# Kernel tuning notes

Measured on AMD Instinct MI355X. Metric: run time of the kernel, lower is better.

## Reference

```python
import jax, jax.numpy as jnp
import numpy as np

B = 256      # graph pairs
NPG = 28     # nodes per graph
MAXN = 32    # max_node_set_size
EPG = 64     # edges per graph (== max_edge_set_size, so no edge padding)
MAXE = 64
D = 128      # node_state_dim
FN = 32      # raw node feature dim
FE = 32      # raw edge feature dim
SK = 64      # sinkhorn_feature_dim
STEPS = 3    # propagation_steps
TEMP = 0.1
ITERS = 20
CW = 0.9     # consistency_weight
G = 2 * B
N = G * NPG
E = G * EPG


def _lin(key, fi, fo):
    return jax.random.normal(key, (fi, fo), jnp.float32) / np.sqrt(fi)


def setup_inputs() -> dict:
    key = jax.random.key(0)
    ks = jax.random.split(key, 12)
    rng = np.random.default_rng(0)
    off = (np.arange(G) * NPG)[:, None]   # graphs ordered q0,c0,q1,c1,...
    from_idx = jnp.asarray((rng.integers(0, NPG, (G, EPG)) + off).reshape(-1), jnp.int32)
    to_idx = jnp.asarray((rng.integers(0, NPG, (G, EPG)) + off).reshape(-1), jnp.int32)
    return dict(
        node_features=jax.random.normal(ks[0], (N, FN), jnp.float32),
        edge_features=jax.random.normal(ks[1], (E, FE), jnp.float32),
        enc_nw=_lin(ks[2], FN, D), enc_nb=jnp.zeros((D,), jnp.float32),
        enc_ew=_lin(ks[3], FE, D), enc_eb=jnp.zeros((D,), jnp.float32),
        msg_w1=_lin(ks[4], 3 * D, 2 * D), msg_b1=jnp.zeros((2 * D,), jnp.float32),
        msg_w2=_lin(ks[5], 2 * D, D), msg_b2=jnp.zeros((D,), jnp.float32),
        rmsg_w1=_lin(ks[6], 3 * D, 2 * D), rmsg_b1=jnp.zeros((2 * D,), jnp.float32),
        rmsg_w2=_lin(ks[7], 2 * D, D), rmsg_b2=jnp.zeros((D,), jnp.float32),
        upd_w1=_lin(ks[8], 2 * D, 2 * D), upd_b1=jnp.zeros((2 * D,), jnp.float32),
        upd_w2=_lin(ks[9], 2 * D, D), upd_b2=jnp.zeros((D,), jnp.float32),
        sk_w1=_lin(ks[10], D, SK), sk_b1=jnp.zeros((SK,), jnp.float32),
        sk_w2=_lin(ks[11], SK, SK), sk_b2=jnp.zeros((SK,), jnp.float32),
        from_idx=from_idx, to_idx=to_idx,
        query_sizes=jnp.full((B,), NPG, jnp.int32),
        corpus_sizes=jnp.full((B,), NPG, jnp.int32),
    )


def _mlp2(x, w1, b1, w2, b2):
    return jnp.maximum(x @ w1 + b1, 0.0) @ w2 + b2


def _sinkhorn(log_alpha):
    # log-domain sinkhorn (noise_factor = 0 -> deterministic)
    la = log_alpha / TEMP
    for _ in range(ITERS):
        la = la - jax.nn.logsumexp(la, axis=2, keepdims=True)
        la = la - jax.nn.logsumexp(la, axis=1, keepdims=True)
    return jnp.exp(la)


def _align(q, c, plan):
    # feature_alignment_score: -relu(q - P @ c).sum over set and feature dims
    return -jnp.maximum(q - plan @ c, 0.0).sum(axis=(1, 2))


def _forward(node_features, edge_features, enc_nw, enc_nb, enc_ew, enc_eb,
             msg_w1, msg_b1, msg_w2, msg_b2, rmsg_w1, rmsg_b1, rmsg_w2, rmsg_b2,
             upd_w1, upd_b1, upd_w2, upd_b2, sk_w1, sk_b1, sk_w2, sk_b2,
             from_idx, to_idx, query_sizes, corpus_sizes):
    h = node_features @ enc_nw + enc_nb        # encoder, [N, D]
    e = edge_features @ enc_ew + enc_eb        # [E, D]

    def messages(h):
        f = _mlp2(jnp.concatenate([h[from_idx], h[to_idx], e], -1), msg_w1, msg_b1, msg_w2, msg_b2)
        r = _mlp2(jnp.concatenate([h[to_idx], h[from_idx], e], -1), rmsg_w1, rmsg_b1, rmsg_w2, rmsg_b2)
        return f, r

    for _ in range(STEPS):  # GraphPropLayer x propagation_steps
        f, r = messages(h)
        agg = jax.ops.segment_sum(f, to_idx, num_segments=N) + \
              jax.ops.segment_sum(r, from_idx, num_segments=N)
        h = h + _mlp2(jnp.concatenate([agg, h], -1), upd_w1, upd_b1, upd_w2, upd_b2)

    # split_and_stack nodes: graphs alternate query/corpus, pad NPG -> MAXN
    hs = jnp.pad(h.reshape(B, 2, NPG, D), ((0, 0), (0, 0), (0, MAXN - NPG), (0, 0)))
    q_nodes, c_nodes = hs[:, 0], hs[:, 1]      # [B, MAXN, D]

    tq = _mlp2(q_nodes, sk_w1, sk_b1, sk_w2, sk_b2)
    tc = _mlp2(c_nodes, sk_w1, sk_b1, sk_w2, sk_b2)
    pos = jnp.arange(MAXN)[None, :]
    mq = tq * (pos < query_sizes[:, None])[..., None]
    mc = tc * (pos < corpus_sizes[:, None])[..., None]
    node_plan = _sinkhorn(jnp.einsum('bqd,bcd->bqc', mq, mc))   # [B, MAXN, MAXN]

    # propagation_messages on final node states
    f, r = messages(h)
    em = (f + r).reshape(B, 2, EPG, D)         # EPG == MAXE -> no pad
    q_edges, c_edges = em[:, 0], em[:, 1]

    # local (within-graph) endpoint indices for kronecker lookup
    fl = (from_idx % NPG).reshape(B, 2, EPG)
    tl = (to_idx % NPG).reshape(B, 2, EPG)
    qf, cf = fl[:, 0], fl[:, 1]
    qt, ct = tl[:, 0], tl[:, 1]

    def kron(T, qf, qt, cf, ct):
        straight = T[qf][:, cf] * T[qt][:, ct]   # [MAXE, MAXE]
        cross = T[qf][:, ct] * T[qt][:, cf]
        return straight + cross

    edge_scores = jax.vmap(kron)(node_plan, qf, qt, cf, ct)     # [B, MAXE, MAXE]
    edge_plan = _sinkhorn(edge_scores)

    return _align(q_nodes, c_nodes, node_plan) + CW * _align(q_edges, c_edges, edge_plan)


def reference(node_features, edge_features, enc_nw, enc_nb, enc_ew, enc_eb,
              msg_w1, msg_b1, msg_w2, msg_b2, rmsg_w1, rmsg_b1, rmsg_w2, rmsg_b2,
              upd_w1, upd_b1, upd_w2, upd_b2, sk_w1, sk_b1, sk_w2, sk_b2,
              from_idx, to_idx, query_sizes, corpus_sizes):
    return _forward(node_features, edge_features, enc_nw, enc_nb, enc_ew, enc_eb,
                    msg_w1, msg_b1, msg_w2, msg_b2, rmsg_w1, rmsg_b1, rmsg_w2, rmsg_b2,
                    upd_w1, upd_b1, upd_w2, upd_b2, sk_w1, sk_b1, sk_w2, sk_b2,
                    from_idx, to_idx, query_sizes, corpus_sizes)
```

## Files before the change

### kernel.cpp

```cpp
#include <hip/hip_runtime.h>
#include <math.h>

#define NPG 28
#define EPG 64
#define NB  256
#define NG  512
#define NN  14336
#define NE  32768
#define TEMPINV 10.0f
#define SINK_ITERS 20
#define CW 0.9f

typedef unsigned int uint;
typedef unsigned short ushort;
typedef __attribute__((ext_vector_type(8))) __bf16 bf16x8;
typedef __attribute__((ext_vector_type(4))) float f32x4;

__device__ __forceinline__ ushort f2bf(float x) {
    uint u = __float_as_uint(x);
    u += 0x7fffu + ((u >> 16) & 1u);
    return (ushort)(u >> 16);
}
__device__ __forceinline__ uint f2bf2(float lo, float hi) {
    return (uint)f2bf(lo) | ((uint)f2bf(hi) << 16);
}
__device__ __forceinline__ float bflo(uint w) { return __uint_as_float(w << 16); }
__device__ __forceinline__ float bfhi(uint w) { return __uint_as_float(w & 0xffff0000u); }
__device__ __forceinline__ uint relu_sum_pk(uint w1, uint w2, uint w3) {
    float lo = fmaxf(bflo(w1) + bflo(w2) + bflo(w3), 0.f);
    float hi = fmaxf(bfhi(w1) + bfhi(w2) + bfhi(w3), 0.f);
    return f2bf2(lo, hi);
}
__device__ __forceinline__ uint4 pack_f32x8(const float* src) {
    const float4 f0 = *(const float4*)src;
    const float4 f1 = *(const float4*)(src + 4);
    uint4 o;
    o.x = f2bf2(f0.x, f0.y);
    o.y = f2bf2(f0.z, f0.w);
    o.z = f2bf2(f1.x, f1.y);
    o.w = f2bf2(f1.z, f1.w);
    return o;
}
__device__ __forceinline__ f32x4 mfma16(bf16x8 a, bf16x8 b, f32x4 c) {
    return __builtin_amdgcn_mfma_f32_16x16x32_bf16(a, b, c, 0, 0, 0);
}

__global__ __launch_bounds__(512, 1) void gnn_fused(
    const float* __restrict__ nf, const float* __restrict__ ef,
    const ushort* __restrict__ encL, const float* __restrict__ enc_nb,
    const ushort* __restrict__ WcombL, const float* __restrict__ bcomb,
    const ushort* __restrict__ WhpL,
    const ushort* __restrict__ W2fL, const ushort* __restrict__ W2rL,
    const float* __restrict__ b2f, const float* __restrict__ b2r,
    const ushort* __restrict__ UW1T, const float* __restrict__ ub1,
    const ushort* __restrict__ UW2T, const float* __restrict__ ub2,
    const int* __restrict__ from_idx, const int* __restrict__ to_idx,
    float* __restrict__ h, float* __restrict__ EM)
{
    __shared__ ushort HPs[NPG * 520];
    __shared__ ushort ECs[2 * 8 * 2048];
    __shared__ float acc_s[NPG * 132];
    __shared__ float hs[NPG * 132];
    __shared__ int fl[64], tl[64];
    const int g = blockIdx.x;
    const int tid = threadIdx.x;
    const int w = tid >> 6, lane = tid & 63;
    const int li = lane & 15, quad = lane >> 4;
    const int wm = w >> 1, wn = w & 1;
    ushort* hid = &HPs[0];

    if (tid < 64) {
        fl[tid] = from_idx[g * 64 + tid] - g * NPG;
        tl[tid] = to_idx[g * 64 + tid] - g * NPG;
    }

    {
        uint4 anf[2];
#pragma unroll
        for (int mi = 0; mi < 2; ++mi) {
            const int row = mi * 16 + li;
            const int rr = (row < NPG) ? row : 0;
            const float4 f0 = *(const float4*)(nf + ((size_t)g * NPG + rr) * 32 + quad * 8);
            const float4 f1 = *(const float4*)(nf + ((size_t)g * NPG + rr) * 32 + quad * 8 + 4);
            uint4 o;
            o.x = f2bf2(f0.x, f0.y); o.y = f2bf2(f0.z, f0.w);
            o.z = f2bf2(f1.x, f1.y); o.w = f2bf2(f1.z, f1.w);
            anf[mi] = o;
        }
        const int col = w * 16 + li;
        const bf16x8 b = __builtin_bit_cast(bf16x8,
            *(const uint4*)(encL + (size_t)col * 32 + quad * 8));
        f32x4 c0 = mfma16(__builtin_bit_cast(bf16x8, anf[0]), b, f32x4{0.f, 0.f, 0.f, 0.f});
        f32x4 c1 = mfma16(__builtin_bit_cast(bf16x8, anf[1]), b, f32x4{0.f, 0.f, 0.f, 0.f});
        const float bv = enc_nb[col];
#pragma unroll
        for (int r = 0; r < 4; ++r) {
            const int r0 = quad * 4 + r;
            hs[r0 * 132 + col] = c0[r] + bv;
            const int r1 = 16 + quad * 4 + r;
            if (r1 < NPG) hs[r1 * 132 + col] = c1[r] + bv;
        }
    }
    {
        uint4 aef[4];
#pragma unroll
        for (int mi = 0; mi < 4; ++mi) {
            const int e = mi * 16 + li;
            const float4 f0 = *(const float4*)(ef + ((size_t)g * 64 + e) * 32 + quad * 8);
            const float4 f1 = *(const float4*)(ef + ((size_t)g * 64 + e) * 32 + quad * 8 + 4);
            uint4 o;
            o.x = f2bf2(f0.x, f0.y); o.y = f2bf2(f0.z, f0.w);
            o.z = f2bf2(f1.x, f1.y); o.w = f2bf2(f1.z, f1.w);
            aef[mi] = o;
        }
#pragma unroll
        for (int ni = 0; ni < 4; ++ni) {
            const int col = w * 64 + ni * 16 + li;
            const bf16x8 b = __builtin_bit_cast(bf16x8,
                *(const uint4*)(WcombL + (size_t)col * 32 + quad * 8));
            const float bv = bcomb[col];
            const int pp = col >> 8, kbl = (col >> 5) & 7, j = col & 31;
#pragma unroll
            for (int mi = 0; mi < 4; ++mi) {
                f32x4 c = mfma16(__builtin_bit_cast(bf16x8, aef[mi]), b,
                                 f32x4{0.f, 0.f, 0.f, 0.f});
#pragma unroll
                for (int r = 0; r < 4; ++r) {
                    const int e = mi * 16 + quad * 4 + r;
                    ECs[pp * 16384 + kbl * 2048 + e * 32 + j] = f2bf(c[r] + bv);
                }
            }
        }
    }
    __syncthreads();

#pragma unroll 1
    for (int step = 0; step < 3; ++step) {
        uint4 ha[2][4];
#pragma unroll
        for (int mi = 0; mi < 2; ++mi) {
            const int row = mi * 16 + li;
            const int rr = (row < NPG) ? row : 0;
#pragma unroll
            for (int kb = 0; kb < 4; ++kb)
                ha[mi][kb] = pack_f32x8(&hs[rr * 132 + kb * 32 + quad * 8]);
        }
        for (int u = tid; u < NPG * 132; u += 512) acc_s[u] = 0.f;

        f32x4 acc[4];
#pragma unroll
        for (int j = 0; j < 4; ++j) acc[j] = f32x4{0.f, 0.f, 0.f, 0.f};

#pragma unroll 1
        for (int p = 0; p < 2; ++p) {
            {
                const int colw = w * 64;
#pragma unroll
                for (int ni = 0; ni < 4; ++ni) {
                    const int col = colw + ni * 16 + li;
                    const ushort* pb = WhpL + (size_t)(p * 512 + col) * 32 + quad * 8;
                    f32x4 c0 = f32x4{0.f, 0.f, 0.f, 0.f};
                    f32x4 c1 = f32x4{0.f, 0.f, 0.f, 0.f};
#pragma unroll
                    for (int kb = 0; kb < 4; ++kb) {
                        const bf16x8 b = __builtin_bit_cast(bf16x8,
                            *(const uint4*)(pb + (size_t)kb * 32768));
                        c0 = mfma16(__builtin_bit_cast(bf16x8, ha[0][kb]), b, c0);
                        c1 = mfma16(__builtin_bit_cast(bf16x8, ha[1][kb]), b, c1);
                    }
#pragma unroll
                    for (int r = 0; r < 4; ++r) {
                        const int r0 = quad * 4 + r;
                        HPs[r0 * 520 + col] = f2bf(c0[r]);
                        const int r1 = 16 + quad * 4 + r;
                        if (r1 < NPG) HPs[r1 * 520 + col] = f2bf(c1[r]);
                    }
                }
            }
            __syncthreads();

            if (p == 1) {
#pragma unroll
                for (int j = 0; j < 4; ++j) acc[j] = f32x4{0.f, 0.f, 0.f, 0.f};
            }
            const int e = wm * 16 + li;
            const int i1 = p ? tl[e] : fl[e];
            const int i2 = p ? fl[e] : tl[e];
            const int ad1 = i1 * 520 + quad * 8;
            const int ad2 = i2 * 520 + 256 + quad * 8;
            const int ade = p * 16384 + e * 32 + quad * 8;
            const ushort* W2L = p ? W2rL : W2fL;
            const int n0 = wn * 64;
            const ushort* pb[4];
#pragma unroll
            for (int ni = 0; ni < 4; ++ni)
                pb[ni] = W2L + (size_t)(n0 + ni * 16 + li) * 32 + quad * 8;
#pragma unroll
            for (int kb = 0; kb < 8; ++kb) {
                const uint4 u1 = *(const uint4*)&HPs[ad1 + kb * 32];
                const uint4 u2 = *(const uint4*)&HPs[ad2 + kb * 32];
                const uint4 ue = *(const uint4*)&ECs[ade + kb * 2048];
                uint4 o;
                o.x = relu_sum_pk(u1.x, u2.x, ue.x);
                o.y = relu_sum_pk(u1.y, u2.y, ue.y);
                o.z = relu_sum_pk(u1.z, u2.z, ue.z);
                o.w = relu_sum_pk(u1.w, u2.w, ue.w);
                const bf16x8 a = __builtin_bit_cast(bf16x8, o);
#pragma unroll
                for (int ni = 0; ni < 4; ++ni) {
                    const bf16x8 b = __builtin_bit_cast(bf16x8,
                        *(const uint4*)(pb[ni] + (size_t)kb * 4096));
                    acc[ni] = mfma16(a, b, acc[ni]);
                }
            }
            {
                const int* targ = p ? fl : tl;
                const float* bias = p ? b2r : b2f;
                float bv[4];
#pragma unroll
                for (int ni = 0; ni < 4; ++ni) bv[ni] = bias[n0 + ni * 16 + li];
#pragma unroll
                for (int r = 0; r < 4; ++r) {
                    const int loc = targ[wm * 16 + quad * 4 + r];
#pragma unroll
                    for (int ni = 0; ni < 4; ++ni)
                        atomicAdd(&acc_s[loc * 132 + n0 + ni * 16 + li],
                                  acc[ni][r] + bv[ni]);
                }
            }
            __syncthreads();
        }

        {
            const int n0u = w * 32;
            f32x4 ua[2][2];
#pragma unroll
            for (int mi = 0; mi < 2; ++mi)
#pragma unroll
                for (int ni = 0; ni < 2; ++ni) ua[mi][ni] = f32x4{0.f, 0.f, 0.f, 0.f};
            const ushort* pb0 = UW1T + (size_t)(n0u + li) * 256 + quad * 8;
            const ushort* pb1 = UW1T + (size_t)(n0u + 16 + li) * 256 + quad * 8;
#pragma unroll
            for (int kb = 0; kb < 8; ++kb) {
                bf16x8 a[2];
                if (kb < 4) {
#pragma unroll
                    for (int mi = 0; mi < 2; ++mi) {
                        const int row = mi * 16 + li;
                        const int rr = (row < NPG) ? row : 0;
                        a[mi] = __builtin_bit_cast(bf16x8,
                            pack_f32x8(&acc_s[rr * 132 + kb * 32 + quad * 8]));
                    }
                } else {
                    a[0] = __builtin_bit_cast(bf16x8, ha[0][kb - 4]);
                    a[1] = __builtin_bit_cast(bf16x8, ha[1][kb - 4]);
                }
                const bf16x8 b0 = __builtin_bit_cast(bf16x8, *(const uint4*)(pb0 + kb * 32));
                const bf16x8 b1 = __builtin_bit_cast(bf16x8, *(const uint4*)(pb1 + kb * 32));
#pragma unroll
                for (int mi = 0; mi < 2; ++mi) {
                    ua[mi][0] = mfma16(a[mi], b0, ua[mi][0]);
                    ua[mi][1] = mfma16(a[mi], b1, ua[mi][1]);
                }
            }
            const float bv0 = ub1[n0u + li], bv1 = ub1[n0u + 16 + li];
#pragma unroll
            for (int mi = 0; mi < 2; ++mi)
#pragma unroll
                for (int r = 0; r < 4; ++r) {
                    const int row = mi * 16 + quad * 4 + r;
                    if (row < NPG) {
                        hid[row * 264 + n0u + li] = f2bf(fmaxf(ua[mi][0][r] + bv0, 0.f));
                        hid[row * 264 + n0u + 16 + li] = f2bf(fmaxf(ua[mi][1][r] + bv1, 0.f));
                    }
                }
        }
        __syncthreads();
        {
            const int n0u = w * 16;
            f32x4 ua[2];
            ua[0] = f32x4{0.f, 0.f, 0.f, 0.f};
            ua[1] = f32x4{0.f, 0.f, 0.f, 0.f};
            const ushort* pb0 = UW2T + (size_t)(n0u + li) * 256 + quad * 8;
#pragma unroll
            for (int kb = 0; kb < 8; ++kb) {
                bf16x8 a[2];
#pragma unroll
                for (int mi = 0; mi < 2; ++mi) {
                    const int row = mi * 16 + li;
                    const int rr = (row < NPG) ? row : 0;
                    a[mi] = __builtin_bit_cast(bf16x8,
                        *(const uint4*)&hid[rr * 264 + kb * 32 + quad * 8]);
                }
                const bf16x8 b0 = __builtin_bit_cast(bf16x8, *(const uint4*)(pb0 + kb * 32));
                ua[0] = mfma16(a[0], b0, ua[0]);
                ua[1] = mfma16(a[1], b0, ua[1]);
            }
            const float bv = ub2[n0u + li];
#pragma unroll
            for (int mi = 0; mi < 2; ++mi)
#pragma unroll
                for (int r = 0; r < 4; ++r) {
                    const int row = mi * 16 + quad * 4 + r;
                    if (row < NPG)
                        hs[row * 132 + n0u + li] += ua[mi][r] + bv;
                }
        }
        __syncthreads();
    }

    {
        uint4 ha[2][4];
#pragma unroll
        for (int mi = 0; mi < 2; ++mi) {
            const int row = mi * 16 + li;
            const int rr = (row < NPG) ? row : 0;
#pragma unroll
            for (int kb = 0; kb < 4; ++kb)
                ha[mi][kb] = pack_f32x8(&hs[rr * 132 + kb * 32 + quad * 8]);
        }
        f32x4 acc[4];
#pragma unroll
        for (int j = 0; j < 4; ++j) acc[j] = f32x4{0.f, 0.f, 0.f, 0.f};
        const int n0 = wn * 64;
#pragma unroll 1
        for (int p = 0; p < 2; ++p) {
            {
                const int colw = w * 64;
#pragma unroll
                for (int ni = 0; ni < 4; ++ni) {
                    const int col = colw + ni * 16 + li;
                    const ushort* pb = WhpL + (size_t)(p * 512 + col) * 32 + quad * 8;
                    f32x4 c0 = f32x4{0.f, 0.f, 0.f, 0.f};
                    f32x4 c1 = f32x4{0.f, 0.f, 0.f, 0.f};
#pragma unroll
                    for (int kb = 0; kb < 4; ++kb) {
                        const bf16x8 b = __builtin_bit_cast(bf16x8,
                            *(const uint4*)(pb + (size_t)kb * 32768));
                        c0 = mfma16(__builtin_bit_cast(bf16x8, ha[0][kb]), b, c0);
                        c1 = mfma16(__builtin_bit_cast(bf16x8, ha[1][kb]), b, c1);
                    }
#pragma unroll
                    for (int r = 0; r < 4; ++r) {
                        const int r0 = quad * 4 + r;
                        HPs[r0 * 520 + col] = f2bf(c0[r]);
                        const int r1 = 16 + quad * 4 + r;
                        if (r1 < NPG) HPs[r1 * 520 + col] = f2bf(c1[r]);
                    }
                }
            }
            __syncthreads();
            const int e = wm * 16 + li;
            const int i1 = p ? tl[e] : fl[e];
            const int i2 = p ? fl[e] : tl[e];
            const int ad1 = i1 * 520 + quad * 8;
            const int ad2 = i2 * 520 + 256 + quad * 8;
            const int ade = p * 16384 + e * 32 + quad * 8;
            const ushort* W2L = p ? W2rL : W2fL;
            const ushort* pb[4];
#pragma unroll
            for (int ni = 0; ni < 4; ++ni)
                pb[ni] = W2L + (size_t)(n0 + ni * 16 + li) * 32 + quad * 8;
#pragma unroll
            for (int kb = 0; kb < 8; ++kb) {
                const uint4 u1 = *(const uint4*)&HPs[ad1 + kb * 32];
                const uint4 u2 = *(const uint4*)&HPs[ad2 + kb * 32];
                const uint4 ue = *(const uint4*)&ECs[ade + kb * 2048];
                uint4 o;
                o.x = relu_sum_pk(u1.x, u2.x, ue.x);
                o.y = relu_sum_pk(u1.y, u2.y, ue.y);
                o.z = relu_sum_pk(u1.z, u2.z, ue.z);
                o.w = relu_sum_pk(u1.w, u2.w, ue.w);
                const bf16x8 a = __builtin_bit_cast(bf16x8, o);
#pragma unroll
                for (int ni = 0; ni < 4; ++ni) {
                    const bf16x8 b = __builtin_bit_cast(bf16x8,
                        *(const uint4*)(pb[ni] + (size_t)kb * 4096));
                    acc[ni] = mfma16(a, b, acc[ni]);
                }
            }
            __syncthreads();
        }
        float bv[4];
#pragma unroll
        for (int ni = 0; ni < 4; ++ni)
            bv[ni] = b2f[n0 + ni * 16 + li] + b2r[n0 + ni * 16 + li];
#pragma unroll
        for (int r = 0; r < 4; ++r) {
            const int erow = g * 64 + wm * 16 + quad * 4 + r;
#pragma unroll
            for (int ni = 0; ni < 4; ++ni)
                EM[(size_t)erow * 128 + n0 + ni * 16 + li] = acc[ni][r] + bv[ni];
        }
    }
    for (int u = tid; u < NPG * 128; u += 512)
        h[(size_t)g * (NPG * 128) + u] = hs[(u >> 7) * 132 + (u & 127)];
}

__global__ __launch_bounds__(256) void pack2(
    const float* __restrict__ msg_w1, const float* __restrict__ rmsg_w1,
    const float* __restrict__ msg_b1, const float* __restrict__ rmsg_b1,
    const float* __restrict__ enc_ew, const float* __restrict__ enc_eb,
    const float* __restrict__ enc_nw,
    const float* __restrict__ msg_w2, const float* __restrict__ rmsg_w2,
    const float* __restrict__ upd_w1, const float* __restrict__ upd_w2,
    ushort* __restrict__ WcombL, float* __restrict__ bcomb,
    ushort* __restrict__ encL,
    ushort* __restrict__ WhpL, ushort* __restrict__ W2fL, ushort* __restrict__ W2rL,
    ushort* __restrict__ UW1T, ushort* __restrict__ UW2T)
{
    const int gid = blockIdx.x, tid = threadIdx.x;
    if (gid < 64) {
        const int idx = gid * 256 + tid;
        const int a = idx >> 9, n = idx & 511;
        const float* Wsrc = (n < 256) ? msg_w1 : rmsg_w1;
        const int nc = n & 255;
        float s = 0.f;
        for (int j = 0; j < 128; ++j)
            s = fmaf(enc_ew[a * 128 + j], Wsrc[(256 + j) * 256 + nc], s);
        WcombL[n * 32 + a] = f2bf(s);
    } else if (gid < 66) {
        const int n = (gid - 64) * 256 + tid;
        const float* Wsrc = (n < 256) ? msg_w1 : rmsg_w1;
        const float* bsrc = (n < 256) ? msg_b1 : rmsg_b1;
        const int nc = n & 255;
        float s = bsrc[nc];
        for (int j = 0; j < 128; ++j)
            s = fmaf(enc_eb[j], Wsrc[(256 + j) * 256 + nc], s);
        bcomb[n] = s;
    } else if (gid < 82) {
        const int idx = (gid - 66) * 256 + tid;
        const int n = idx >> 5, k = idx & 31;
        encL[idx] = f2bf(enc_nw[k * 128 + n]);
    } else if (gid < 594) {
        const int idx = (gid - 82) * 256 + tid;
        const int n = idx >> 7, k = idx & 127;
        const float* Wsrc = (n < 512) ? msg_w1 : rmsg_w1;
        const int part = (n >> 8) & 1, col = n & 255;
        WhpL[(size_t)(k >> 5) * 32768 + n * 32 + (k & 31)] =
            f2bf(Wsrc[(part * 128 + k) * 256 + col]);
    } else if (gid < 722) {
        const int idx = (gid - 594) * 256 + tid;
        const int n = idx >> 8, k = idx & 255;
        W2fL[(size_t)(k >> 5) * 4096 + n * 32 + (k & 31)] = f2bf(msg_w2[k * 128 + n]);
    } else if (gid < 850) {
        const int idx = (gid - 722) * 256 + tid;
        const int n = idx >> 8, k = idx & 255;
        W2rL[(size_t)(k >> 5) * 4096 + n * 32 + (k & 31)] = f2bf(rmsg_w2[k * 128 + n]);
    } else if (gid < 1106) {
        const int idx = (gid - 850) * 256 + tid;
        const int n = idx >> 8, k = idx & 255;
        UW1T[idx] = f2bf(upd_w1[k * 256 + n]);
    } else {
        const int idx = (gid - 1106) * 256 + tid;
        const int n = idx >> 8, k = idx & 255;
        UW2T[idx] = f2bf(upd_w2[k * 128 + n]);
    }
}

__global__ __launch_bounds__(256) void node_kernel(
    const float* __restrict__ h,
    const float* __restrict__ w1, const float* __restrict__ b1,
    const float* __restrict__ w2, const float* __restrict__ b2,
    const int* __restrict__ qsz, const int* __restrict__ csz,
    float* __restrict__ plan_out, float* __restrict__ loss_out)
{
    __shared__ float qn[32][128];
    __shared__ float cn[32][128];
    __shared__ float t1[32][64];
    __shared__ float mq[32][68];
    __shared__ float mc[32][68];
    __shared__ float la[32][33];
    __shared__ float red[4];
    const int bb = blockIdx.x;
    const int tid = threadIdx.x;
    const int qs = qsz[bb], cs = csz[bb];
    for (int u = tid * 4; u < 4096; u += 1024) {
        const int p = u >> 7, d = u & 127;
        float4 zq = make_float4(0.f, 0.f, 0.f, 0.f), zc = zq;
        if (p < NPG) {
            zq = *(const float4*)(h + (size_t)((2 * bb) * NPG + p) * 128 + d);
            zc = *(const float4*)(h + (size_t)((2 * bb + 1) * NPG + p) * 128 + d);
        }
        *(float4*)&qn[p][d] = zq;
        *(float4*)&cn[p][d] = zc;
    }
    __syncthreads();
    const int col = tid & 63;
    const int rg  = tid >> 6;
    for (int s = 0; s < 2; ++s) {
        const float (*src)[128] = s ? cn : qn;
        float (*dst)[68] = s ? mc : mq;
        const int sz = s ? cs : qs;
        float a8[8];
#pragma unroll
        for (int u = 0; u < 8; ++u) a8[u] = b1[col];
        for (int k = 0; k < 128; ++k) {
            const float wv = w1[k * 64 + col];
#pragma unroll
            for (int u = 0; u < 8; ++u) a8[u] = fmaf(src[rg + 4 * u][k], wv, a8[u]);
        }
#pragma unroll
        for (int u = 0; u < 8; ++u) t1[rg + 4 * u][col] = fmaxf(a8[u], 0.f);
        __syncthreads();
#pragma unroll
        for (int u = 0; u < 8; ++u) a8[u] = b2[col];
        for (int k = 0; k < 64; ++k) {
            const float wv = w2[k * 64 + col];
#pragma unroll
            for (int u = 0; u < 8; ++u) a8[u] = fmaf(t1[rg + 4 * u][k], wv, a8[u]);
        }
#pragma unroll
        for (int u = 0; u < 8; ++u) {
            const int r = rg + 4 * u;
            dst[r][col] = (r < sz) ? a8[u] : 0.f;
        }
        __syncthreads();
    }
    {
        const int q = tid >> 3, cg = tid & 7;
#pragma unroll
        for (int u = 0; u < 4; ++u) {
            const int c = cg + 8 * u;
            float s = 0.f;
            for (int d = 0; d < 64; ++d) s = fmaf(mq[q][d], mc[c][d], s);
            la[q][c] = s * TEMPINV;
        }
    }
    __syncthreads();
    const int l8 = tid & 7, rq = tid >> 3;
    for (int it = 0; it < SINK_ITERS; ++it) {
        {
            float x[4];
#pragma unroll
            for (int u = 0; u < 4; ++u) x[u] = la[rq][l8 * 4 + u];
            float m = fmaxf(fmaxf(x[0], x[1]), fmaxf(x[2], x[3]));
            m = fmaxf(m, __shfl_xor(m, 1));
            m = fmaxf(m, __shfl_xor(m, 2));
            m = fmaxf(m, __shfl_xor(m, 4));
            float s = __expf(x[0] - m) + __expf(x[1] - m) + __expf(x[2] - m) + __expf(x[3] - m);
            s += __shfl_xor(s, 1);
            s += __shfl_xor(s, 2);
            s += __shfl_xor(s, 4);
            const float lse = m + __logf(s);
#pragma unroll
            for (int u = 0; u < 4; ++u) la[rq][l8 * 4 + u] = x[u] - lse;
        }
        __syncthreads();
        {
            float x[4];
#pragma unroll
            for (int u = 0; u < 4; ++u) x[u] = la[l8 * 4 + u][rq];
            float m = fmaxf(fmaxf(x[0], x[1]), fmaxf(x[2], x[3]));
            m = fmaxf(m, __shfl_xor(m, 1));
            m = fmaxf(m, __shfl_xor(m, 2));
            m = fmaxf(m, __shfl_xor(m, 4));
            float s = __expf(x[0] - m) + __expf(x[1] - m) + __expf(x[2] - m) + __expf(x[3] - m);
            s += __shfl_xor(s, 1);
            s += __shfl_xor(s, 2);
            s += __shfl_xor(s, 4);
            const float lse = m + __logf(s);
#pragma unroll
            for (int u = 0; u < 4; ++u) la[l8 * 4 + u][rq] = x[u] - lse;
        }
        __syncthreads();
    }
    for (int u = tid; u < 1024; u += 256) {
        const int q = u >> 5, c = u & 31;
        const float p = __expf(la[q][c]);
        la[q][c] = p;
        plan_out[(size_t)bb * 1024 + u] = p;
    }
    __syncthreads();
    float lsum = 0.f;
    {
        const int q = tid >> 3, dg = tid & 7;
        for (int u = 0; u < 16; ++u) {
            const int d = dg + 8 * u;
            float pc = 0.f;
#pragma unroll
            for (int c = 0; c < 32; ++c) pc = fmaf(la[q][c], cn[c][d], pc);
            lsum += fmaxf(qn[q][d] - pc, 0.f);
        }
    }
#pragma unroll
    for (int off = 1; off < 64; off <<= 1) lsum += __shfl_xor(lsum, off);
    if ((tid & 63) == 0) red[tid >> 6] = lsum;
    __syncthreads();
    if (tid == 0) loss_out[bb] = -(red[0] + red[1] + red[2] + red[3]);
}

__global__ __launch_bounds__(256) void edge_kernel(
    const float* __restrict__ plan, const float* __restrict__ EM,
    const int* __restrict__ from_idx, const int* __restrict__ to_idx,
    float* __restrict__ loss_out)
{
    __shared__ float T[32][33];
    __shared__ float la[64][65];
    __shared__ float ce[64][128];
    __shared__ int qf[64], qt[64], cfi[64], cti[64];
    __shared__ float red[4];
    const int bb = blockIdx.x;
    const int tid = threadIdx.x;
    for (int u = tid; u < 1024; u += 256) T[u >> 5][u & 31] = plan[(size_t)bb * 1024 + u];
    if (tid < 64) {
        const int gq = 2 * bb, gc = 2 * bb + 1;
        qf[tid]  = from_idx[gq * 64 + tid] - gq * NPG;
        qt[tid]  = to_idx  [gq * 64 + tid] - gq * NPG;
        cfi[tid] = from_idx[gc * 64 + tid] - gc * NPG;
        cti[tid] = to_idx  [gc * 64 + tid] - gc * NPG;
    }
    {
        const int gc = 2 * bb + 1;
        for (int u = tid * 4; u < 8192; u += 1024) {
            const int i = u >> 7, d = u & 127;
            *(float4*)&ce[i][d] = *(const float4*)(EM + (size_t)(gc * 64 + i) * 128 + d);
        }
    }
    __syncthreads();
    {
        const int i = tid >> 2, jg = tid & 3;
        const int a = qf[i], b_ = qt[i];
#pragma unroll
        for (int u = 0; u < 16; ++u) {
            const int j = jg * 16 + u;
            const float s = T[a][cfi[j]] * T[b_][cti[j]] + T[a][cti[j]] * T[b_][cfi[j]];
            la[i][j] = s * TEMPINV;
        }
    }
    __syncthreads();
    const int l4 = tid & 3, rr = tid >> 2;
    for (int it = 0; it < SINK_ITERS; ++it) {
        {
            float x[16];
#pragma unroll
            for (int u = 0; u < 16; ++u) x[u] = la[rr][l4 * 16 + u];
            float m = x[0];
#pragma unroll
            for (int u = 1; u < 16; ++u) m = fmaxf(m, x[u]);
            m = fmaxf(m, __shfl_xor(m, 1));
            m = fmaxf(m, __shfl_xor(m, 2));
            float s = 0.f;
#pragma unroll
            for (int u = 0; u < 16; ++u) s += __expf(x[u] - m);
            s += __shfl_xor(s, 1);
            s += __shfl_xor(s, 2);
            const float lse = m + __logf(s);
#pragma unroll
            for (int u = 0; u < 16; ++u) la[rr][l4 * 16 + u] = x[u] - lse;
        }
        __syncthreads();
        {
            float x[16];
#pragma unroll
            for (int u = 0; u < 16; ++u) x[u] = la[l4 * 16 + u][rr];
            float m = x[0];
#pragma unroll
            for (int u = 1; u < 16; ++u) m = fmaxf(m, x[u]);
            m = fmaxf(m, __shfl_xor(m, 1));
            m = fmaxf(m, __shfl_xor(m, 2));
            float s = 0.f;
#pragma unroll
            for (int u = 0; u < 16; ++u) s += __expf(x[u] - m);
            s += __shfl_xor(s, 1);
            s += __shfl_xor(s, 2);
            const float lse = m + __logf(s);
#pragma unroll
            for (int u = 0; u < 16; ++u) la[l4 * 16 + u][rr] = x[u] - lse;
        }
        __syncthreads();
    }
    for (int u = tid; u < 4096; u += 256) la[u >> 6][u & 63] = __expf(la[u >> 6][u & 63]);
    __syncthreads();
    float lsum = 0.f;
    {
        const int q = tid >> 2, dg = tid & 3;
        const float* qe = EM + (size_t)((2 * bb) * 64 + q) * 128;
        for (int u = 0; u < 32; ++u) {
            const int d = dg + 4 * u;
            float pc = 0.f;
            for (int c = 0; c < 64; ++c) pc = fmaf(la[q][c], ce[c][d], pc);
            lsum += fmaxf(qe[d] - pc, 0.f);
        }
    }
#pragma unroll
    for (int off = 1; off < 64; off <<= 1) lsum += __shfl_xor(lsum, off);
    if ((tid & 63) == 0) red[tid >> 6] = lsum;
    __syncthreads();
    if (tid == 0) loss_out[bb] -= CW * (red[0] + red[1] + red[2] + red[3]);
}

extern "C" void kernel_launch(void* const* d_in, const int* in_sizes, int n_in,
                              void* d_out, int out_size, void* d_ws, size_t ws_size,
                              hipStream_t stream)
{
    const float* node_features = (const float*)d_in[0];
    const float* edge_features = (const float*)d_in[1];
    const float* enc_nw  = (const float*)d_in[2];
    const float* enc_nb  = (const float*)d_in[3];
    const float* enc_ew  = (const float*)d_in[4];
    const float* enc_eb  = (const float*)d_in[5];
    const float* msg_w1  = (const float*)d_in[6];
    const float* msg_b1  = (const float*)d_in[7];
    const float* msg_w2  = (const float*)d_in[8];
    const float* msg_b2  = (const float*)d_in[9];
    const float* rmsg_w1 = (const float*)d_in[10];
    const float* rmsg_b1 = (const float*)d_in[11];
    const float* rmsg_w2 = (const float*)d_in[12];
    const float* rmsg_b2 = (const float*)d_in[13];
    const float* upd_w1  = (const float*)d_in[14];
    const float* upd_b1  = (const float*)d_in[15];
    const float* upd_w2  = (const float*)d_in[16];
    const float* upd_b2  = (const float*)d_in[17];
    const float* sk_w1   = (const float*)d_in[18];
    const float* sk_b1   = (const float*)d_in[19];
    const float* sk_w2   = (const float*)d_in[20];
    const float* sk_b2   = (const float*)d_in[21];
    const int* from_idx  = (const int*)d_in[22];
    const int* to_idx    = (const int*)d_in[23];
    const int* qsizes    = (const int*)d_in[24];
    const int* csizes    = (const int*)d_in[25];
    float* out = (float*)d_out;

    float* ws     = (float*)d_ws;
    float* h      = ws;
    float* EM     = h + (size_t)NN * 128;
    float* plan   = EM + (size_t)NE * 128;
    float* bcomb  = plan + (size_t)NB * 1024;
    ushort* WcombL = (ushort*)(bcomb + 512);
    ushort* encL  = WcombL + 16384;
    ushort* WhpL  = encL + 4096;
    ushort* W2fL  = WhpL + 131072;
    ushort* W2rL  = W2fL + 32768;
    ushort* UW1T  = W2rL + 32768;
    ushort* UW2T  = UW1T + 65536;

    const dim3 blk(256);
    const dim3 blk512(512);

    pack2<<<1234, blk, 0, stream>>>(msg_w1, rmsg_w1, msg_b1, rmsg_b1,
                                    enc_ew, enc_eb, enc_nw, msg_w2, rmsg_w2,
                                    upd_w1, upd_w2,
                                    WcombL, bcomb, encL, WhpL, W2fL, W2rL, UW1T, UW2T);

    gnn_fused<<<dim3(NG), blk512, 0, stream>>>(
        node_features, edge_features, encL, enc_nb, WcombL, bcomb,
        WhpL, W2fL, W2rL, msg_b2, rmsg_b2,
        UW1T, upd_b1, UW2T, upd_b2, from_idx, to_idx, h, EM);

    node_kernel<<<NB, blk, 0, stream>>>(
        h, sk_w1, sk_b1, sk_w2, sk_b2, qsizes, csizes, plan, out);
    edge_kernel<<<NB, blk, 0, stream>>>(
        plan, EM, from_idx, to_idx, out);
}
```

Before: 467.5 us.

## Halve fused GNN block to 256 threads and keep edge-encoder output in registers

The fused GNN kernel now runs 256 threads per graph instead of 512, with each wave covering twice as many output columns, and launch bounds are set to allow two blocks per CU. The edge-encoder projections no longer sit in a dedicated 64KB shared buffer. They are computed through the reused HPs buffer and loaded once into per-thread registers (ecf) for all propagation steps. The aim is to cut shared memory use so more blocks fit per CU and to drop repeated LDS reads of edge terms. The cost is more registers per thread (8 accumulators plus 16 uint4 of edge data) and less parallelism within each block.

```diff
diff --git a/kernel.cpp b/kernel.cpp
--- a/kernel.cpp
+++ b/kernel.cpp
@@ -45,7 +45,7 @@
     return __builtin_amdgcn_mfma_f32_16x16x32_bf16(a, b, c, 0, 0, 0);
 }
 
-__global__ __launch_bounds__(512, 1) void gnn_fused(
+__global__ __launch_bounds__(256, 2) void gnn_fused(
     const float* __restrict__ nf, const float* __restrict__ ef,
     const ushort* __restrict__ encL, const float* __restrict__ enc_nb,
     const ushort* __restrict__ WcombL, const float* __restrict__ bcomb,
@@ -57,8 +57,7 @@
     const int* __restrict__ from_idx, const int* __restrict__ to_idx,
     float* __restrict__ h, float* __restrict__ EM)
 {
-    __shared__ ushort HPs[NPG * 520];
-    __shared__ ushort ECs[2 * 8 * 2048];
+    __shared__ ushort HPs[16640];
     __shared__ float acc_s[NPG * 132];
     __shared__ float hs[NPG * 132];
     __shared__ int fl[64], tl[64];
@@ -66,7 +65,6 @@
     const int tid = threadIdx.x;
     const int w = tid >> 6, lane = tid & 63;
     const int li = lane & 15, quad = lane >> 4;
-    const int wm = w >> 1, wn = w & 1;
     ushort* hid = &HPs[0];
 
     if (tid < 64) {
@@ -87,20 +85,25 @@
             o.z = f2bf2(f1.x, f1.y); o.w = f2bf2(f1.z, f1.w);
             anf[mi] = o;
         }
-        const int col = w * 16 + li;
-        const bf16x8 b = __builtin_bit_cast(bf16x8,
-            *(const uint4*)(encL + (size_t)col * 32 + quad * 8));
-        f32x4 c0 = mfma16(__builtin_bit_cast(bf16x8, anf[0]), b, f32x4{0.f, 0.f, 0.f, 0.f});
-        f32x4 c1 = mfma16(__builtin_bit_cast(bf16x8, anf[1]), b, f32x4{0.f, 0.f, 0.f, 0.f});
-        const float bv = enc_nb[col];
-#pragma unroll
-        for (int r = 0; r < 4; ++r) {
-            const int r0 = quad * 4 + r;
-            hs[r0 * 132 + col] = c0[r] + bv;
-            const int r1 = 16 + quad * 4 + r;
-            if (r1 < NPG) hs[r1 * 132 + col] = c1[r] + bv;
-        }
-    }
+#pragma unroll
+        for (int ni = 0; ni < 2; ++ni) {
+            const int col = w * 32 + ni * 16 + li;
+            const bf16x8 b = __builtin_bit_cast(bf16x8,
+                *(const uint4*)(encL + (size_t)col * 32 + quad * 8));
+            f32x4 c0 = mfma16(__builtin_bit_cast(bf16x8, anf[0]), b, f32x4{0.f, 0.f, 0.f, 0.f});
+            f32x4 c1 = mfma16(__builtin_bit_cast(bf16x8, anf[1]), b, f32x4{0.f, 0.f, 0.f, 0.f});
+            const float bv = enc_nb[col];
+#pragma unroll
+            for (int r = 0; r < 4; ++r) {
+                const int r0 = quad * 4 + r;
+                hs[r0 * 132 + col] = c0[r] + bv;
+                const int r1 = 16 + quad * 4 + r;
+                if (r1 < NPG) hs[r1 * 132 + col] = c1[r] + bv;
+            }
+        }
+    }
+
+    uint4 ecf[2][8];
     {
         uint4 aef[4];
 #pragma unroll
@@ -113,26 +116,35 @@
             o.z = f2bf2(f1.x, f1.y); o.w = f2bf2(f1.z, f1.w);
             aef[mi] = o;
         }
-#pragma unroll
-        for (int ni = 0; ni < 4; ++ni) {
-            const int col = w * 64 + ni * 16 + li;
-            const bf16x8 b = __builtin_bit_cast(bf16x8,
-                *(const uint4*)(WcombL + (size_t)col * 32 + quad * 8));
-            const float bv = bcomb[col];
-            const int pp = col >> 8, kbl = (col >> 5) & 7, j = col & 31;
-#pragma unroll
-            for (int mi = 0; mi < 4; ++mi) {
-                f32x4 c = mfma16(__builtin_bit_cast(bf16x8, aef[mi]), b,
-                                 f32x4{0.f, 0.f, 0.f, 0.f});
-#pragma unroll
-                for (int r = 0; r < 4; ++r) {
-                    const int e = mi * 16 + quad * 4 + r;
-                    ECs[pp * 16384 + kbl * 2048 + e * 32 + j] = f2bf(c[r] + bv);
-                }
-            }
-        }
-    }
-    __syncthreads();
+#pragma unroll 1
+        for (int p = 0; p < 2; ++p) {
+#pragma unroll
+            for (int ni = 0; ni < 4; ++ni) {
+                const int col = w * 64 + ni * 16 + li;
+                const int wcol = p * 256 + col;
+                const bf16x8 b = __builtin_bit_cast(bf16x8,
+                    *(const uint4*)(WcombL + (size_t)wcol * 32 + quad * 8));
+                const float bv = bcomb[wcol];
+                const int kbl = col >> 5, j = col & 31;
+#pragma unroll
+                for (int mi = 0; mi < 4; ++mi) {
+                    f32x4 c = mfma16(__builtin_bit_cast(bf16x8, aef[mi]), b,
+                                     f32x4{0.f, 0.f, 0.f, 0.f});
+#pragma unroll
+                    for (int r = 0; r < 4; ++r) {
+                        const int e = mi * 16 + quad * 4 + r;
+                        HPs[kbl * 2048 + e * 32 + j] = f2bf(c[r] + bv);
+                    }
+                }
+            }
+            __syncthreads();
+            const int eb = (w * 16 + li) * 32 + quad * 8;
+#pragma unroll
+            for (int kb = 0; kb < 8; ++kb)
+                ecf[p][kb] = *(const uint4*)&HPs[kb * 2048 + eb];
+            __syncthreads();
+        }
+    }
 
 #pragma unroll 1
     for (int step = 0; step < 3; ++step) {
@@ -145,18 +157,14 @@
             for (int kb = 0; kb < 4; ++kb)
                 ha[mi][kb] = pack_f32x8(&hs[rr * 132 + kb * 32 + quad * 8]);
         }
-        for (int u = tid; u < NPG * 132; u += 512) acc_s[u] = 0.f;
-
-        f32x4 acc[4];
-#pragma unroll
-        for (int j = 0; j < 4; ++j) acc[j] = f32x4{0.f, 0.f, 0.f, 0.f};
+        for (int u = tid; u < NPG * 132; u += 256) acc_s[u] = 0.f;
 
 #pragma unroll 1
         for (int p = 0; p < 2; ++p) {
             {
-                const int colw = w * 64;
-#pragma unroll
-                for (int ni = 0; ni < 4; ++ni) {
+                const int colw = w * 128;
+#pragma unroll
+                for (int ni = 0; ni < 8; ++ni) {
                     const int col = colw + ni * 16 + li;
                     const ushort* pb = WhpL + (size_t)(p * 512 + col) * 32 + quad * 8;
                     f32x4 c0 = f32x4{0.f, 0.f, 0.f, 0.f};
@@ -179,27 +187,20 @@
             }
             __syncthreads();
 
-            if (p == 1) {
-#pragma unroll
-                for (int j = 0; j < 4; ++j) acc[j] = f32x4{0.f, 0.f, 0.f, 0.f};
-            }
-            const int e = wm * 16 + li;
+            const int e = w * 16 + li;
             const int i1 = p ? tl[e] : fl[e];
             const int i2 = p ? fl[e] : tl[e];
             const int ad1 = i1 * 520 + quad * 8;
             const int ad2 = i2 * 520 + 256 + quad * 8;
-            const int ade = p * 16384 + e * 32 + quad * 8;
             const ushort* W2L = p ? W2rL : W2fL;
-            const int n0 = wn * 64;
-            const ushort* pb[4];
-#pragma unroll
-            for (int ni = 0; ni < 4; ++ni)
-                pb[ni] = W2L + (size_t)(n0 + ni * 16 + li) * 32 + quad * 8;
+            f32x4 acc[8];
+#pragma unroll
+            for (int j = 0; j < 8; ++j) acc[j] = f32x4{0.f, 0.f, 0.f, 0.f};
 #pragma unroll
             for (int kb = 0; kb < 8; ++kb) {
                 const uint4 u1 = *(const uint4*)&HPs[ad1 + kb * 32];
                 const uint4 u2 = *(const uint4*)&HPs[ad2 + kb * 32];
-                const uint4 ue = *(const uint4*)&ECs[ade + kb * 2048];
+                const uint4 ue = ecf[p][kb];
                 uint4 o;
                 o.x = relu_sum_pk(u1.x, u2.x, ue.x);
                 o.y = relu_sum_pk(u1.y, u2.y, ue.y);
@@ -207,24 +208,25 @@
                 o.w = relu_sum_pk(u1.w, u2.w, ue.w);
                 const bf16x8 a = __builtin_bit_cast(bf16x8, o);
 #pragma unroll
-                for (int ni = 0; ni < 4; ++ni) {
+                for (int ni = 0; ni < 8; ++ni) {
                     const bf16x8 b = __builtin_bit_cast(bf16x8,
-                        *(const uint4*)(pb[ni] + (size_t)kb * 4096));
+                        *(const uint4*)(W2L + (size_t)(ni * 16 + li) * 32 +
+                                        quad * 8 + (size_t)kb * 4096));
                     acc[ni] = mfma16(a, b, acc[ni]);
                 }
             }
             {
                 const int* targ = p ? fl : tl;
                 const float* bias = p ? b2r : b2f;
-                float bv[4];
-#pragma unroll
-                for (int ni = 0; ni < 4; ++ni) bv[ni] = bias[n0 + ni * 16 + li];
+                float bv[8];
+#pragma unroll
+                for (int ni = 0; ni < 8; ++ni) bv[ni] = bias[ni * 16 + li];
 #pragma unroll
                 for (int r = 0; r < 4; ++r) {
-                    const int loc = targ[wm * 16 + quad * 4 + r];
-#pragma unroll
-                    for (int ni = 0; ni < 4; ++ni)
-                        atomicAdd(&acc_s[loc * 132 + n0 + ni * 16 + li],
+                    const int loc = targ[w * 16 + quad * 4 + r];
+#pragma unroll
+                    for (int ni = 0; ni < 8; ++ni)
+                        atomicAdd(&acc_s[loc * 132 + ni * 16 + li],
                                   acc[ni][r] + bv[ni]);
                 }
             }
@@ -232,14 +234,16 @@
         }
 
         {
-            const int n0u = w * 32;
-            f32x4 ua[2][2];
+            const int n0u = w * 64;
+            f32x4 ua[2][4];
 #pragma unroll
             for (int mi = 0; mi < 2; ++mi)
 #pragma unroll
-                for (int ni = 0; ni < 2; ++ni) ua[mi][ni] = f32x4{0.f, 0.f, 0.f, 0.f};
-            const ushort* pb0 = UW1T + (size_t)(n0u + li) * 256 + quad * 8;
-            const ushort* pb1 = UW1T + (size_t)(n0u + 16 + li) * 256 + quad * 8;
+                for (int ni = 0; ni < 4; ++ni) ua[mi][ni] = f32x4{0.f, 0.f, 0.f, 0.f};
+            const ushort* pb[4];
+#pragma unroll
+            for (int ni = 0; ni < 4; ++ni)
+                pb[ni] = UW1T + (size_t)(n0u + ni * 16 + li) * 256 + quad * 8;
 #pragma unroll
             for (int kb = 0; kb < 8; ++kb) {
                 bf16x8 a[2];
@@ -255,33 +259,39 @@
                     a[0] = __builtin_bit_cast(bf16x8, ha[0][kb - 4]);
                     a[1] = __builtin_bit_cast(bf16x8, ha[1][kb - 4]);
                 }
-                const bf16x8 b0 = __builtin_bit_cast(bf16x8, *(const uint4*)(pb0 + kb * 32));
-                const bf16x8 b1 = __builtin_bit_cast(bf16x8, *(const uint4*)(pb1 + kb * 32));
-#pragma unroll
-                for (int mi = 0; mi < 2; ++mi) {
-                    ua[mi][0] = mfma16(a[mi], b0, ua[mi][0]);
-                    ua[mi][1] = mfma16(a[mi], b1, ua[mi][1]);
-                }
-            }
-            const float bv0 = ub1[n0u + li], bv1 = ub1[n0u + 16 + li];
-#pragma unroll
-            for (int mi = 0; mi < 2; ++mi)
-#pragma unroll
-                for (int r = 0; r < 4; ++r) {
-                    const int row = mi * 16 + quad * 4 + r;
-                    if (row < NPG) {
-                        hid[row * 264 + n0u + li] = f2bf(fmaxf(ua[mi][0][r] + bv0, 0.f));
-                        hid[row * 264 + n0u + 16 + li] = f2bf(fmaxf(ua[mi][1][r] + bv1, 0.f));
+#pragma unroll
+                for (int ni = 0; ni < 4; ++ni) {
+                    const bf16x8 b = __builtin_bit_cast(bf16x8,
+                        *(const uint4*)(pb[ni] + kb * 32));
+#pragma unroll
+                    for (int mi = 0; mi < 2; ++mi)
+                        ua[mi][ni] = mfma16(a[mi], b, ua[mi][ni]);
+                }
+            }
+#pragma unroll
+            for (int ni = 0; ni < 4; ++ni) {
+                const float bv = ub1[n0u + ni * 16 + li];
+#pragma unroll
+                for (int mi = 0; mi < 2; ++mi)
+#pragma unroll
+                    for (int r = 0; r < 4; ++r) {
+                        const int row = mi * 16 + quad * 4 + r;
+                        if (row < NPG)
+                            hid[row * 264 + n0u + ni * 16 + li] =
+                                f2bf(fmaxf(ua[mi][ni][r] + bv, 0.f));
                     }
-                }
+            }
         }
         __syncthreads();
         {
-            const int n0u = w * 16;
-            f32x4 ua[2];
-            ua[0] = f32x4{0.f, 0.f, 0.f, 0.f};
-            ua[1] = f32x4{0.f, 0.f, 0.f, 0.f};
+            const int n0u = w * 32;
+            f32x4 ua[2][2];
+#pragma unroll
+            for (int mi = 0; mi < 2; ++mi)
+#pragma unroll
+                for (int ni = 0; ni < 2; ++ni) ua[mi][ni] = f32x4{0.f, 0.f, 0.f, 0.f};
             const ushort* pb0 = UW2T + (size_t)(n0u + li) * 256 + quad * 8;
+            const ushort* pb1 = UW2T + (size_t)(n0u + 16 + li) * 256 + quad * 8;
 #pragma unroll
             for (int kb = 0; kb < 8; ++kb) {
                 bf16x8 a[2];
@@ -293,17 +303,23 @@
                         *(const uint4*)&hid[rr * 264 + kb * 32 + quad * 8]);
                 }
                 const bf16x8 b0 = __builtin_bit_cast(bf16x8, *(const uint4*)(pb0 + kb * 32));
-                ua[0] = mfma16(a[0], b0, ua[0]);
-                ua[1] = mfma16(a[1], b0, ua[1]);
-            }
-            const float bv = ub2[n0u + li];
+                const bf16x8 b1 = __builtin_bit_cast(bf16x8, *(const uint4*)(pb1 + kb * 32));
+#pragma unroll
+                for (int mi = 0; mi < 2; ++mi) {
+                    ua[mi][0] = mfma16(a[mi], b0, ua[mi][0]);
+                    ua[mi][1] = mfma16(a[mi], b1, ua[mi][1]);
+                }
+            }
+            const float bv0 = ub2[n0u + li], bv1 = ub2[n0u + 16 + li];
 #pragma unroll
             for (int mi = 0; mi < 2; ++mi)
 #pragma unroll
                 for (int r = 0; r < 4; ++r) {
                     const int row = mi * 16 + quad * 4 + r;
-                    if (row < NPG)
-                        hs[row * 132 + n0u + li] += ua[mi][r] + bv;
+                    if (row < NPG) {
+                        hs[row * 132 + n0u + li] += ua[mi][0][r] + bv0;
+                        hs[row * 132 + n0u + 16 + li] += ua[mi][1][r] + bv1;
+                    }
                 }
         }
         __syncthreads();
@@ -319,16 +335,15 @@
             for (int kb = 0; kb < 4; ++kb)
                 ha[mi][kb] = pack_f32x8(&hs[rr * 132 + kb * 32 + quad * 8]);
         }
-        f32x4 acc[4];
-#pragma unroll
-        for (int j = 0; j < 4; ++j) acc[j] = f32x4{0.f, 0.f, 0.f, 0.f};
-        const int n0 = wn * 64;
+        f32x4 acc[8];
+#pragma unroll
+        for (int j = 0; j < 8; ++j) acc[j] = f32x4{0.f, 0.f, 0.f, 0.f};
 #pragma unroll 1
         for (int p = 0; p < 2; ++p) {
             {
-                const int colw = w * 64;
-#pragma unroll
-                for (int ni = 0; ni < 4; ++ni) {
+                const int colw = w * 128;
+#pragma unroll
+                for (int ni = 0; ni < 8; ++ni) {
                     const int col = colw + ni * 16 + li;
                     const ushort* pb = WhpL + (size_t)(p * 512 + col) * 32 + quad * 8;
                     f32x4 c0 = f32x4{0.f, 0.f, 0.f, 0.f};
@@ -350,22 +365,17 @@
                 }
             }
             __syncthreads();
-            const int e = wm * 16 + li;
+            const int e = w * 16 + li;
             const int i1 = p ? tl[e] : fl[e];
             const int i2 = p ? fl[e] : tl[e];
             const int ad1 = i1 * 520 + quad * 8;
             const int ad2 = i2 * 520 + 256 + quad * 8;
-            const int ade = p * 16384 + e * 32 + quad * 8;
             const ushort* W2L = p ? W2rL : W2fL;
-            const ushort* pb[4];
-#pragma unroll
-            for (int ni = 0; ni < 4; ++ni)
-                pb[ni] = W2L + (size_t)(n0 + ni * 16 + li) * 32 + quad * 8;
 #pragma unroll
             for (int kb = 0; kb < 8; ++kb) {
                 const uint4 u1 = *(const uint4*)&HPs[ad1 + kb * 32];
                 const uint4 u2 = *(const uint4*)&HPs[ad2 + kb * 32];
-                const uint4 ue = *(const uint4*)&ECs[ade + kb * 2048];
+                const uint4 ue = ecf[p][kb];
                 uint4 o;
                 o.x = relu_sum_pk(u1.x, u2.x, ue.x);
                 o.y = relu_sum_pk(u1.y, u2.y, ue.y);
@@ -373,27 +383,27 @@
                 o.w = relu_sum_pk(u1.w, u2.w, ue.w);
                 const bf16x8 a = __builtin_bit_cast(bf16x8, o);
 #pragma unroll
-                for (int ni = 0; ni < 4; ++ni) {
+                for (int ni = 0; ni < 8; ++ni) {
                     const bf16x8 b = __builtin_bit_cast(bf16x8,
-                        *(const uint4*)(pb[ni] + (size_t)kb * 4096));
+                        *(const uint4*)(W2L + (size_t)(ni * 16 + li) * 32 +
+                                        quad * 8 + (size_t)kb * 4096));
                     acc[ni] = mfma16(a, b, acc[ni]);
                 }
             }
             __syncthreads();
         }
-        float bv[4];
-#pragma unroll
-        for (int ni = 0; ni < 4; ++ni)
-            bv[ni] = b2f[n0 + ni * 16 + li] + b2r[n0 + ni * 16 + li];
-#pragma unroll
-        for (int r = 0; r < 4; ++r) {
-            const int erow = g * 64 + wm * 16 + quad * 4 + r;
-#pragma unroll
-            for (int ni = 0; ni < 4; ++ni)
-                EM[(size_t)erow * 128 + n0 + ni * 16 + li] = acc[ni][r] + bv[ni];
-        }
-    }
-    for (int u = tid; u < NPG * 128; u += 512)
+#pragma unroll
+        for (int ni = 0; ni < 8; ++ni) {
+            const int c = ni * 16 + li;
+            const float bv = b2f[c] + b2r[c];
+#pragma unroll
+            for (int r = 0; r < 4; ++r) {
+                const int erow = g * 64 + w * 16 + quad * 4 + r;
+                EM[(size_t)erow * 128 + c] = acc[ni][r] + bv;
+            }
+        }
+    }
+    for (int u = tid; u < NPG * 128; u += 256)
         h[(size_t)g * (NPG * 128) + u] = hs[(u >> 7) * 132 + (u & 127)];
 }
 
@@ -736,14 +746,13 @@
     ushort* UW2T  = UW1T + 65536;
 
     const dim3 blk(256);
-    const dim3 blk512(512);
 
     pack2<<<1234, blk, 0, stream>>>(msg_w1, rmsg_w1, msg_b1, rmsg_b1,
                                     enc_ew, enc_eb, enc_nw, msg_w2, rmsg_w2,
                                     upd_w1, upd_w2,
                                     WcombL, bcomb, encL, WhpL, W2fL, W2rL, UW1T, UW2T);
 
-    gnn_fused<<<dim3(NG), blk512, 0, stream>>>(
+    gnn_fused<<<dim3(NG), blk, 0, stream>>>(
         node_features, edge_features, encL, enc_nb, WcombL, bcomb,
         WhpL, W2fL, W2rL, msg_b2, rmsg_b2,
         UW1T, upd_b1, UW2T, upd_b2, from_idx, to_idx, h, EM);
```

Measured after the change: 554.1 us. +18.5%, slower.
